# Kernel optimization log

Measured on AMD Instinct MI355X. Metric: run time of the kernel, lower is better.

The kernel has to match this reference:

```python
import jax, jax.numpy as jnp
import numpy as np
from jax import lax

B, T, I = 64, 128, 128   # batch, encoder time, signal features
H = 512                  # lstm hidden size
V = 32                   # vocab = len(output_dict); SOS=0, EOS=1
L = 64                   # decode steps = target_onehot.shape[1]


def lstm_cell(x, h, c, Wih, Whh, bih, bhh):
    # PyTorch gate order: i, f, g, o. x:[B,in], h/c:[B,H]
    g = x @ Wih.T + h @ Whh.T + (bih + bhh)
    i, f, gg, o = jnp.split(g, 4, axis=-1)
    c_new = jax.nn.sigmoid(f) * c + jax.nn.sigmoid(i) * jnp.tanh(gg)
    h_new = jax.nn.sigmoid(o) * jnp.tanh(c_new)
    return h_new, c_new


def setup_inputs() -> dict:
    key = jax.random.key(0)
    ks = jax.random.split(key, 16)
    s = 1.0 / np.sqrt(H)
    u = lambda k, shape: jax.random.uniform(k, shape, jnp.float32, -s, s)
    inp = {}
    inp["signal"] = jax.random.normal(ks[0], (B, T, I), jnp.float32)
    tgt_ids = jax.random.randint(ks[1], (B, L), 0, V)
    inp["target_onehot"] = jax.nn.one_hot(tgt_ids, V, dtype=jnp.float32)
    # encoder bi-LSTM params, stacked [2(dir), ...]
    inp["enc_Wih"] = u(ks[2], (2, 4 * H, I))
    inp["enc_Whh"] = u(ks[3], (2, 4 * H, H))
    inp["enc_bih"] = u(ks[4], (2, 4 * H))
    inp["enc_bhh"] = u(ks[5], (2, 4 * H))
    # decoder bi-LSTM params
    inp["dec_Wih"] = u(ks[6], (2, 4 * H, V))
    inp["dec_Whh"] = u(ks[7], (2, 4 * H, H))
    inp["dec_bih"] = u(ks[8], (2, 4 * H))
    inp["dec_bhh"] = u(ks[9], (2, 4 * H))
    # output projection Linear(2H -> V)
    so = 1.0 / np.sqrt(2 * H)
    inp["W_out"] = jax.random.uniform(ks[10], (V, 2 * H), jnp.float32, -so, so)
    inp["b_out"] = jax.random.uniform(ks[11], (V,), jnp.float32, -so, so)
    return inp


def _forward(signal, target_onehot, enc_Wih, enc_Whh, enc_bih, enc_bhh,
             dec_Wih, dec_Whh, dec_bih, dec_bhh, W_out, b_out):
    Bv = signal.shape[0]
    zeros = jnp.zeros((Bv, H), signal.dtype)
    xs = jnp.swapaxes(signal, 0, 1)  # [T,B,I]

    def enc_step(d):
        def f(carry, x):
            h, c = carry
            h, c = lstm_cell(x, h, c, enc_Wih[d], enc_Whh[d], enc_bih[d], enc_bhh[d])
            return (h, c), None
        return f

    # forward direction final state; backward direction runs on reversed seq
    (hf, cf), _ = lax.scan(enc_step(0), (zeros, zeros), xs)
    (hb, cb), _ = lax.scan(enc_step(1), (zeros, zeros), xs[::-1])

    def dec_step(carry, _):
        inp, hf, cf, hb, cb = carry
        x = jax.nn.relu(inp)  # relu of one-hot (identity, kept for fidelity)
        hf, cf = lstm_cell(x, hf, cf, dec_Wih[0], dec_Whh[0], dec_bih[0], dec_bhh[0])
        hb, cb = lstm_cell(x, hb, cb, dec_Wih[1], dec_Whh[1], dec_bih[1], dec_bhh[1])
        logits = jnp.concatenate([hf, hb], axis=-1) @ W_out.T + b_out  # [B,V]
        # teacher forcing prob is 0 in the source -> always greedy one-hot feedback
        nxt = jax.nn.one_hot(jnp.argmax(logits, axis=-1), V, dtype=logits.dtype)
        return (nxt, hf, cf, hb, cb), logits

    init = (target_onehot[:, 0], hf, cf, hb, cb)
    _, logits = lax.scan(dec_step, init, None, length=target_onehot.shape[1])
    logits = jnp.swapaxes(logits, 0, 1)  # [B,L,V]
    return jax.nn.log_softmax(logits, axis=-1)


def reference(signal, target_onehot, enc_Wih, enc_Whh, enc_bih, enc_bhh,
              dec_Wih, dec_Whh, dec_bih, dec_bhh, W_out, b_out):
    return _forward(signal, target_onehot, enc_Wih, enc_Whh, enc_bih, enc_bhh,
                    dec_Wih, dec_Whh, dec_bih, dec_bhh, W_out, b_out)
```

## Files before the change

### kernel.cpp

```cpp
#include <hip/hip_runtime.h>
#include <math.h>

#define DEV __device__ __forceinline__
typedef __attribute__((ext_vector_type(4))) float f32x4;

constexpr int BATCH = 64;
constexpr int TSTEP = 128;
constexpr int IDIM  = 128;
constexpr int HDIM  = 512;
constexpr int VDIM  = 32;
constexpr int LDEC  = 64;
constexpr int NBLK  = 256;
constexpr int BDIM  = 256;
constexpr unsigned MAGIC = 0x1357BD1u;
constexpr unsigned SPIN_LIMIT = 1u << 22;

constexpr size_t OFF_BAR  = 0;
constexpr size_t OFF_SIGT = 4096;
constexpr size_t OFF_HT   = OFF_SIGT + (size_t)TSTEP*IDIM*BATCH*4;
constexpr size_t OFF_XD   = OFF_HT   + (size_t)2*2*HDIM*BATCH*4;
constexpr size_t WS_NEED  = OFF_XD   + (size_t)VDIM*BATCH*4;


DEV unsigned ldu(const unsigned* p){ return __hip_atomic_load(p, __ATOMIC_RELAXED, __HIP_MEMORY_SCOPE_AGENT); }
DEV void     stu(unsigned* p, unsigned v){ __hip_atomic_store(p, v, __ATOMIC_RELAXED, __HIP_MEMORY_SCOPE_AGENT); }
DEV unsigned fau(unsigned* p, unsigned v){ return __hip_atomic_fetch_add(p, v, __ATOMIC_RELAXED, __HIP_MEMORY_SCOPE_AGENT); }
DEV void     ast(float* p, float v){ __hip_atomic_store(p, v, __ATOMIC_RELAXED, __HIP_MEMORY_SCOPE_AGENT); }
DEV void wait_vm0(){ asm volatile("s_waitcnt vmcnt(0)" ::: "memory"); }
DEV f32x4 gl4_sc1(const float* p){ f32x4 r; asm volatile("global_load_dwordx4 %0, %1, off sc1" : "=v"(r) : "v"(p)); return r; }
DEV f32x4 gl4_pln(const float* p){ f32x4 r; asm volatile("global_load_dwordx4 %0, %1, off"     : "=v"(r) : "v"(p)); return r; }
DEV float gl1_sc1(const float* p){ float r; asm volatile("global_load_dword %0, %1, off sc1"   : "=v"(r) : "v"(p)); return r; }

DEV void spin_ge(const unsigned* p, unsigned tgt, unsigned* dead) {
  unsigned spins = 0;
  while (ldu(p) < tgt) {
    __builtin_amdgcn_s_sleep(1);
    if ((++spins & 255u) == 0u) {
      if (ldu(dead)) break;
      if (spins > SPIN_LIMIT) { stu(dead, 1u); break; }
    }
  }
}

DEV void hbar(unsigned* bar, int gline, int grp, int ngrp, unsigned grpsz, int genline, unsigned* dead) {
  wait_vm0();
  __syncthreads();
  if (threadIdx.x == 0) {
    unsigned* gen = bar + genline*32;
    unsigned g = ldu(gen);
    unsigned* gc = bar + (gline + grp)*32;
    unsigned a = fau(gc, 1u);
    bool rel = false;
    if (a == grpsz - 1u) {
      stu(gc, 0u);
      unsigned* rt = bar + (gline + ngrp)*32;
      unsigned ra = fau(rt, 1u);
      if (ra == (unsigned)ngrp - 1u) { stu(rt, 0u); fau(gen, 1u); rel = true; }
    }
    if (!rel) spin_ge(gen, g + 1u, dead);
  }
  __syncthreads();
}

DEV void gbar_full(unsigned* cnt, unsigned* gen, unsigned nb, unsigned* dead) {
  __syncthreads();
  if (threadIdx.x == 0) {
    unsigned g = ldu(gen);
    unsigned a = __hip_atomic_fetch_add(cnt, 1u, __ATOMIC_ACQ_REL, __HIP_MEMORY_SCOPE_AGENT);
    if (a >= nb - 1u) {
      stu(cnt, 0u);
      __hip_atomic_fetch_add(gen, 1u, __ATOMIC_RELEASE, __HIP_MEMORY_SCOPE_AGENT);
    } else {
      spin_ge(gen, g + 1u, dead);
      (void)__hip_atomic_load(gen, __ATOMIC_ACQUIRE, __HIP_MEMORY_SCOPE_AGENT);
    }
  }
  __syncthreads();
}

template<int KX, bool XSC1>
DEV void cell_step(float acc[4], const float* __restrict__ xsrc,
                   const float* __restrict__ hcur,
                   const float* const* wx, const float* const* wh,
                   int b, int tid, float* __restrict__ buf)
{
  constexpr int  NXC = KX / 64;
  constexpr bool XR  = (KX % 64) != 0;
  constexpr int  NC  = NXC + (XR ? 1 : 0) + HDIM / 64;
  f32x4 r[4];

  auto issue = [&](int c) {
    if (c < NXC) {
      const float* s = xsrc + (size_t)c*4096 + tid*4;
      #pragma unroll
      for (int q = 0; q < 4; ++q) r[q] = XSC1 ? gl4_sc1(s + q*1024) : gl4_pln(s + q*1024);
    } else if (XR && c == NXC) {
      const float* s = xsrc + tid*4;
      #pragma unroll
      for (int q = 0; q < 2; ++q) r[q] = XSC1 ? gl4_sc1(s + q*1024) : gl4_pln(s + q*1024);
    } else {
      const int ch = c - NXC - (XR ? 1 : 0);
      const float* s = hcur + (size_t)ch*4096 + tid*4;
      #pragma unroll
      for (int q = 0; q < 4; ++q) r[q] = gl4_sc1(s + q*1024);
    }
  };

  issue(0);
  for (int c = 0; c < NC; ++c) {
    wait_vm0();
    float* dst = buf + (c & 1)*4096;
    const bool small = (XR && c == NXC);
    *(f32x4*)(dst + tid*4)        = r[0];
    *(f32x4*)(dst + tid*4 + 1024) = r[1];
    if (!small) {
      *(f32x4*)(dst + tid*4 + 2048) = r[2];
      *(f32x4*)(dst + tid*4 + 3072) = r[3];
    }
    __syncthreads();
    if (c + 1 < NC) issue(c + 1);
    const float *g0, *g1, *g2, *g3;
    if (c < NXC)            { g0=wx[0]+c*64; g1=wx[1]+c*64; g2=wx[2]+c*64; g3=wx[3]+c*64; }
    else if (XR && c==NXC)  { g0=wx[0];      g1=wx[1];      g2=wx[2];      g3=wx[3]; }
    else { const int ch=c-NXC-(XR?1:0); g0=wh[0]+ch*64; g1=wh[1]+ch*64; g2=wh[2]+ch*64; g3=wh[3]+ch*64; }
    const float* bs = dst + b;
    if (!small) {
      #pragma unroll
      for (int kk = 0; kk < 64; ++kk) {
        float xv = bs[kk*64];
        acc[0] += g0[kk]*xv; acc[1] += g1[kk]*xv; acc[2] += g2[kk]*xv; acc[3] += g3[kk]*xv;
      }
    } else {
      #pragma unroll
      for (int kk = 0; kk < 32; ++kk) {
        float xv = bs[kk*64];
        acc[0] += g0[kk]*xv; acc[1] += g1[kk]*xv; acc[2] += g2[kk]*xv; acc[3] += g3[kk]*xv;
      }
    }
  }
}

__global__ void __launch_bounds__(BDIM)
encdec(const float* __restrict__ signal, const float* __restrict__ tgt,
       const float* __restrict__ eWih, const float* __restrict__ eWhh,
       const float* __restrict__ eBih, const float* __restrict__ eBhh,
       const float* __restrict__ dWih, const float* __restrict__ dWhh,
       const float* __restrict__ dBih, const float* __restrict__ dBhh,
       const float* __restrict__ Wout, const float* __restrict__ bOut,
       float* __restrict__ out,
       unsigned* __restrict__ bar, float* __restrict__ sigT,
       float* __restrict__ hT, float* __restrict__ xdT)
{
  __shared__ __align__(16) float buf[2*4096];
  __shared__ float red[BDIM];
  const int blk = blockIdx.x, tid = threadIdx.x;
  const int d  = blk >> 7;
  const int js = blk & 127;
  const int b  = tid & 63;
  const int jj = tid >> 6;
  const int j  = js * 4 + jj;

  unsigned* dead = bar + 11*32;
  if (blk == 0 && tid == 0) {
    for (int q = 1; q <= 30; ++q) stu(bar + q*32, 0u);
    __hip_atomic_store(bar, MAGIC, __ATOMIC_RELEASE, __HIP_MEMORY_SCOPE_AGENT);
  }
  if (tid == 0) {
    unsigned spins = 0;
    while (__hip_atomic_load(bar, __ATOMIC_RELAXED, __HIP_MEMORY_SCOPE_AGENT) != MAGIC) {
      __builtin_amdgcn_s_sleep(1);
      if (++spins > SPIN_LIMIT) break;
    }
    (void)__hip_atomic_load(bar, __ATOMIC_ACQUIRE, __HIP_MEMORY_SCOPE_AGENT);
  }
  __syncthreads();

  {
    const int t = blk & 127, ih = blk >> 7;
    float* tile = buf;
    for (int idx = tid; idx < 64*64; idx += BDIM) {
      int il = idx & 63, bb = idx >> 6;
      tile[il*65 + bb] = signal[((size_t)bb*TSTEP + t)*IDIM + ih*64 + il];
    }
    __syncthreads();
    for (int idx = tid; idx < 64*64; idx += BDIM) {
      int bb = idx & 63, il = idx >> 6;
      sigT[((size_t)t*IDIM + ih*64 + il)*64 + bb] = tile[il*65 + bb];
    }
  }
  ast(&hT[((size_t)(0*2 + d)*HDIM + j)*64 + b], 0.f);
  ast(&hT[((size_t)(1*2 + d)*HDIM + j)*64 + b], 0.f);
  if (blk < BATCH && tid < VDIM) {
    float tv = tgt[((size_t)blk*LDEC)*VDIM + tid];
    ast(&xdT[tid*64 + blk], tv > 0.f ? tv : 0.f);
  }
  gbar_full(bar + 29*32, bar + 30*32, NBLK, dead);

  const float* wx[4]; const float* wh[4]; float bsum[4];
  #pragma unroll
  for (int g = 0; g < 4; ++g) {
    int r = __builtin_amdgcn_readfirstlane(g*HDIM + j);
    wx[g] = eWih + ((size_t)d*4*HDIM + r)*IDIM;
    wh[g] = eWhh + ((size_t)d*4*HDIM + r)*HDIM;
    bsum[g] = eBih[d*4*HDIM + r] + eBhh[d*4*HDIM + r];
  }
  float c = 0.f;
  for (int t = 0; t < TSTEP; ++t) {
    const int cur = t & 1, nxt = cur ^ 1;
    const int td = d ? (TSTEP - 1 - t) : t;
    float acc[4] = {0.f, 0.f, 0.f, 0.f};
    cell_step<IDIM, false>(acc, sigT + (size_t)td*IDIM*64,
                           hT + ((size_t)(cur*2 + d)*HDIM)*64, wx, wh, b, tid, buf);
    float gi = acc[0]+bsum[0], gf = acc[1]+bsum[1], gg = acc[2]+bsum[2], go = acc[3]+bsum[3];
    float si = 1.f/(1.f+expf(-gi)), sf = 1.f/(1.f+expf(-gf)), so = 1.f/(1.f+expf(-go));
    c = sf*c + si*tanhf(gg);
    ast(&hT[((size_t)(nxt*2 + d)*HDIM + j)*64 + b], so*tanhf(c));
    hbar(bar, d ? 18 : 12, (blk >> 5) & 3, 4, 32u, d ? 23 : 17, dead);
  }
  hbar(bar, 1, blk & 7, 8, 32u, 10, dead);

  #pragma unroll
  for (int g = 0; g < 4; ++g) {
    int r = __builtin_amdgcn_readfirstlane(g*HDIM + j);
    wx[g] = dWih + ((size_t)d*4*HDIM + r)*VDIM;
    wh[g] = dWhh + ((size_t)d*4*HDIM + r)*HDIM;
    bsum[g] = dBih[d*4*HDIM + r] + dBhh[d*4*HDIM + r];
  }
  for (int s = 0; s < LDEC; ++s) {
    const int cur = s & 1, nxt = cur ^ 1;
    float acc[4] = {0.f, 0.f, 0.f, 0.f};
    cell_step<VDIM, true>(acc, xdT, hT + ((size_t)(cur*2 + d)*HDIM)*64, wx, wh, b, tid, buf);
    float gi = acc[0]+bsum[0], gf = acc[1]+bsum[1], gg = acc[2]+bsum[2], go = acc[3]+bsum[3];
    float si = 1.f/(1.f+expf(-gi)), sf = 1.f/(1.f+expf(-gf)), so = 1.f/(1.f+expf(-go));
    c = sf*c + si*tanhf(gg);
    ast(&hT[((size_t)(nxt*2 + d)*HDIM + j)*64 + b], so*tanhf(c));
    hbar(bar, 1, blk & 7, 8, 32u, 10, dead);

    if (blk < BATCH) {
      const int bb = blk, v = tid & 31, kc = tid >> 5;
      const float* hx = hT + (size_t)nxt*2*HDIM*64 + bb;
      float part = 0.f;
      float rr[32];
      for (int w = 0; w < 4; ++w) {
        #pragma unroll
        for (int i = 0; i < 32; ++i)
          rr[i] = gl1_sc1(hx + (size_t)(kc*128 + w*32 + i)*64);
        wait_vm0();
        #pragma unroll
        for (int i = 0; i < 32; ++i)
          part += Wout[(size_t)v*(2*HDIM) + kc*128 + w*32 + i] * rr[i];
      }
      red[tid] = part;
      __syncthreads();
      if (tid < VDIM) {
        float lg = red[tid];
        #pragma unroll
        for (int q = 1; q < 8; ++q) lg += red[tid + q*32];
        lg += bOut[tid];
        float m = lg; int mi = tid;
        #pragma unroll
        for (int off = 16; off >= 1; off >>= 1) {
          float om = __shfl_xor(m, off, 64);
          int omi  = __shfl_xor(mi, off, 64);
          if (om > m || (om == m && omi < mi)) { m = om; mi = omi; }
        }
        float ex = expf(lg - m), ssum = ex;
        #pragma unroll
        for (int off = 16; off >= 1; off >>= 1) ssum += __shfl_xor(ssum, off, 64);
        out[((size_t)bb*LDEC + s)*VDIM + tid] = lg - m - logf(ssum);
        ast(&xdT[tid*64 + bb], (tid == mi) ? 1.f : 0.f);
      }
    }
    hbar(bar, 1, blk & 7, 8, 32u, 10, dead);
  }
}

extern "C" void kernel_launch(void* const* d_in, const int* in_sizes, int n_in,
                              void* d_out, int out_size, void* d_ws, size_t ws_size,
                              hipStream_t stream) {
  if (ws_size < WS_NEED) return;
  char* base = (char*)d_ws;
  hipLaunchKernelGGL(encdec, dim3(NBLK), dim3(BDIM), 0, stream,
    (const float*)d_in[0],  (const float*)d_in[1],
    (const float*)d_in[2],  (const float*)d_in[3],
    (const float*)d_in[4],  (const float*)d_in[5],
    (const float*)d_in[6],  (const float*)d_in[7],
    (const float*)d_in[8],  (const float*)d_in[9],
    (const float*)d_in[10], (const float*)d_in[11],
    (float*)d_out,
    (unsigned*)(base + OFF_BAR), (float*)(base + OFF_SIGT),
    (float*)(base + OFF_HT),     (float*)(base + OFF_XD));
}
```

Before: 4.670 ms.

## Stage per-block LSTM weight slices in LDS and shrink staging chunks

Each block now copies its 16 gate rows of the input and recurrent weights (encoder, then decoder) into shared memory once, with a padded stride. The inner loop then reads weights as vectorized LDS loads instead of per-step global loads through wave-uniform pointers. The input/hidden staging chunk is cut from 64 to 32 k-values, which halves the double buffer and doubles the number of chunk iterations and __syncthreads per step. Shared memory use grows to about 57 KB, which costs one-time copy work and may limit residency.

Result: faster. 4.157 ms (-11.0%).

```diff
diff --git a/kernel.cpp b/kernel.cpp
--- a/kernel.cpp
+++ b/kernel.cpp
@@ -14,6 +14,10 @@
 constexpr int BDIM  = 256;
 constexpr unsigned MAGIC = 0x1357BD1u;
 constexpr unsigned SPIN_LIMIT = 1u << 22;
+
+constexpr int WS_E = 644;
+constexpr int WS_D = 548;
+constexpr int SM_BUF = 0, SM_W = 4096, SM_RED = 4096 + 10304, SM_TOT = 14656;
 
 constexpr size_t OFF_BAR  = 0;
 constexpr size_t OFF_SIGT = 4096;
@@ -78,64 +82,42 @@
   __syncthreads();
 }
 
-template<int KX, bool XSC1>
+template<int KX, int WS, bool XSC1>
 DEV void cell_step(float acc[4], const float* __restrict__ xsrc,
-                   const float* __restrict__ hcur,
-                   const float* const* wx, const float* const* wh,
-                   int b, int tid, float* __restrict__ buf)
+                   const float* __restrict__ hcur, const float* __restrict__ Wl,
+                   int b, int jj, int tid, float* __restrict__ buf)
 {
-  constexpr int  NXC = KX / 64;
-  constexpr bool XR  = (KX % 64) != 0;
-  constexpr int  NC  = NXC + (XR ? 1 : 0) + HDIM / 64;
-  f32x4 r[4];
-
+  constexpr int NXC = KX / 32;
+  constexpr int NC  = NXC + HDIM / 32;
+  f32x4 r0, r1;
   auto issue = [&](int c) {
-    if (c < NXC) {
-      const float* s = xsrc + (size_t)c*4096 + tid*4;
-      #pragma unroll
-      for (int q = 0; q < 4; ++q) r[q] = XSC1 ? gl4_sc1(s + q*1024) : gl4_pln(s + q*1024);
-    } else if (XR && c == NXC) {
-      const float* s = xsrc + tid*4;
-      #pragma unroll
-      for (int q = 0; q < 2; ++q) r[q] = XSC1 ? gl4_sc1(s + q*1024) : gl4_pln(s + q*1024);
-    } else {
-      const int ch = c - NXC - (XR ? 1 : 0);
-      const float* s = hcur + (size_t)ch*4096 + tid*4;
-      #pragma unroll
-      for (int q = 0; q < 4; ++q) r[q] = gl4_sc1(s + q*1024);
-    }
+    const float* s = (c < NXC) ? xsrc + (size_t)c*2048 + tid*8
+                               : hcur + (size_t)(c - NXC)*2048 + tid*8;
+    if (c < NXC && !XSC1) { r0 = gl4_pln(s); r1 = gl4_pln(s + 4); }
+    else                  { r0 = gl4_sc1(s); r1 = gl4_sc1(s + 4); }
   };
-
   issue(0);
   for (int c = 0; c < NC; ++c) {
     wait_vm0();
-    float* dst = buf + (c & 1)*4096;
-    const bool small = (XR && c == NXC);
-    *(f32x4*)(dst + tid*4)        = r[0];
-    *(f32x4*)(dst + tid*4 + 1024) = r[1];
-    if (!small) {
-      *(f32x4*)(dst + tid*4 + 2048) = r[2];
-      *(f32x4*)(dst + tid*4 + 3072) = r[3];
-    }
+    float* dst = buf + (c & 1)*2048;
+    *(f32x4*)(dst + tid*8)     = r0;
+    *(f32x4*)(dst + tid*8 + 4) = r1;
     __syncthreads();
     if (c + 1 < NC) issue(c + 1);
-    const float *g0, *g1, *g2, *g3;
-    if (c < NXC)            { g0=wx[0]+c*64; g1=wx[1]+c*64; g2=wx[2]+c*64; g3=wx[3]+c*64; }
-    else if (XR && c==NXC)  { g0=wx[0];      g1=wx[1];      g2=wx[2];      g3=wx[3]; }
-    else { const int ch=c-NXC-(XR?1:0); g0=wh[0]+ch*64; g1=wh[1]+ch*64; g2=wh[2]+ch*64; g3=wh[3]+ch*64; }
+    const float* wr = Wl + (size_t)(jj*4)*WS + c*32;
     const float* bs = dst + b;
-    if (!small) {
-      #pragma unroll
-      for (int kk = 0; kk < 64; ++kk) {
-        float xv = bs[kk*64];
-        acc[0] += g0[kk]*xv; acc[1] += g1[kk]*xv; acc[2] += g2[kk]*xv; acc[3] += g3[kk]*xv;
-      }
-    } else {
-      #pragma unroll
-      for (int kk = 0; kk < 32; ++kk) {
-        float xv = bs[kk*64];
-        acc[0] += g0[kk]*xv; acc[1] += g1[kk]*xv; acc[2] += g2[kk]*xv; acc[3] += g3[kk]*xv;
-      }
+    #pragma unroll
+    for (int kq = 0; kq < 8; ++kq) {
+      f32x4 w0 = *(const f32x4*)(wr + 0*WS + kq*4);
+      f32x4 w1 = *(const f32x4*)(wr + 1*WS + kq*4);
+      f32x4 w2 = *(const f32x4*)(wr + 2*WS + kq*4);
+      f32x4 w3 = *(const f32x4*)(wr + 3*WS + kq*4);
+      float x0 = bs[(kq*4+0)*64], x1 = bs[(kq*4+1)*64];
+      float x2 = bs[(kq*4+2)*64], x3 = bs[(kq*4+3)*64];
+      acc[0] += w0[0]*x0 + w0[1]*x1 + w0[2]*x2 + w0[3]*x3;
+      acc[1] += w1[0]*x0 + w1[1]*x1 + w1[2]*x2 + w1[3]*x3;
+      acc[2] += w2[0]*x0 + w2[1]*x1 + w2[2]*x2 + w2[3]*x3;
+      acc[3] += w3[0]*x0 + w3[1]*x1 + w3[2]*x2 + w3[3]*x3;
     }
   }
 }
@@ -151,8 +133,10 @@
        unsigned* __restrict__ bar, float* __restrict__ sigT,
        float* __restrict__ hT, float* __restrict__ xdT)
 {
-  __shared__ __align__(16) float buf[2*4096];
-  __shared__ float red[BDIM];
+  __shared__ __align__(16) float smem[SM_TOT];
+  float* buf = smem + SM_BUF;
+  float* Wl  = smem + SM_W;
+  float* red = smem + SM_RED;
   const int blk = blockIdx.x, tid = threadIdx.x;
   const int d  = blk >> 7;
   const int js = blk & 127;
@@ -177,7 +161,7 @@
 
   {
     const int t = blk & 127, ih = blk >> 7;
-    float* tile = buf;
+    float* tile = smem;
     for (int idx = tid; idx < 64*64; idx += BDIM) {
       int il = idx & 63, bb = idx >> 6;
       tile[il*65 + bb] = signal[((size_t)bb*TSTEP + t)*IDIM + ih*64 + il];
@@ -187,6 +171,14 @@
       int bb = idx & 63, il = idx >> 6;
       sigT[((size_t)t*IDIM + ih*64 + il)*64 + bb] = tile[il*65 + bb];
     }
+    __syncthreads();
+  }
+  for (int idx = tid; idx < 16*640; idx += BDIM) {
+    int row = idx / 640, k = idx - row*640;
+    int g = row & 3, ju = row >> 2;
+    int r = d*4*HDIM + g*HDIM + (js*4 + ju);
+    Wl[(size_t)row*WS_E + k] = (k < IDIM) ? eWih[(size_t)r*IDIM + k]
+                                          : eWhh[(size_t)r*HDIM + (k - IDIM)];
   }
   ast(&hT[((size_t)(0*2 + d)*HDIM + j)*64 + b], 0.f);
   ast(&hT[((size_t)(1*2 + d)*HDIM + j)*64 + b], 0.f);
@@ -196,21 +188,19 @@
   }
   gbar_full(bar + 29*32, bar + 30*32, NBLK, dead);
 
-  const float* wx[4]; const float* wh[4]; float bsum[4];
+  float bsum[4];
   #pragma unroll
   for (int g = 0; g < 4; ++g) {
-    int r = __builtin_amdgcn_readfirstlane(g*HDIM + j);
-    wx[g] = eWih + ((size_t)d*4*HDIM + r)*IDIM;
-    wh[g] = eWhh + ((size_t)d*4*HDIM + r)*HDIM;
-    bsum[g] = eBih[d*4*HDIM + r] + eBhh[d*4*HDIM + r];
+    int r = __builtin_amdgcn_readfirstlane(d*4*HDIM + g*HDIM + j);
+    bsum[g] = eBih[r] + eBhh[r];
   }
   float c = 0.f;
   for (int t = 0; t < TSTEP; ++t) {
     const int cur = t & 1, nxt = cur ^ 1;
     const int td = d ? (TSTEP - 1 - t) : t;
     float acc[4] = {0.f, 0.f, 0.f, 0.f};
-    cell_step<IDIM, false>(acc, sigT + (size_t)td*IDIM*64,
-                           hT + ((size_t)(cur*2 + d)*HDIM)*64, wx, wh, b, tid, buf);
+    cell_step<IDIM, WS_E, false>(acc, sigT + (size_t)td*IDIM*64,
+                                 hT + ((size_t)(cur*2 + d)*HDIM)*64, Wl, b, jj, tid, buf);
     float gi = acc[0]+bsum[0], gf = acc[1]+bsum[1], gg = acc[2]+bsum[2], go = acc[3]+bsum[3];
     float si = 1.f/(1.f+expf(-gi)), sf = 1.f/(1.f+expf(-gf)), so = 1.f/(1.f+expf(-go));
     c = sf*c + si*tanhf(gg);
@@ -219,17 +209,25 @@
   }
   hbar(bar, 1, blk & 7, 8, 32u, 10, dead);
 
+  for (int idx = tid; idx < 16*544; idx += BDIM) {
+    int row = idx / 544, k = idx - row*544;
+    int g = row & 3, ju = row >> 2;
+    int r = d*4*HDIM + g*HDIM + (js*4 + ju);
+    Wl[(size_t)row*WS_D + k] = (k < VDIM) ? dWih[(size_t)r*VDIM + k]
+                                          : dWhh[(size_t)r*HDIM + (k - VDIM)];
+  }
   #pragma unroll
   for (int g = 0; g < 4; ++g) {
-    int r = __builtin_amdgcn_readfirstlane(g*HDIM + j);
-    wx[g] = dWih + ((size_t)d*4*HDIM + r)*VDIM;
-    wh[g] = dWhh + ((size_t)d*4*HDIM + r)*HDIM;
-    bsum[g] = dBih[d*4*HDIM + r] + dBhh[d*4*HDIM + r];
-  }
+    int r = __builtin_amdgcn_readfirstlane(d*4*HDIM + g*HDIM + j);
+    bsum[g] = dBih[r] + dBhh[r];
+  }
+  __syncthreads();
+
   for (int s = 0; s < LDEC; ++s) {
     const int cur = s & 1, nxt = cur ^ 1;
     float acc[4] = {0.f, 0.f, 0.f, 0.f};
-    cell_step<VDIM, true>(acc, xdT, hT + ((size_t)(cur*2 + d)*HDIM)*64, wx, wh, b, tid, buf);
+    cell_step<VDIM, WS_D, true>(acc, xdT, hT + ((size_t)(cur*2 + d)*HDIM)*64,
+                                Wl, b, jj, tid, buf);
     float gi = acc[0]+bsum[0], gf = acc[1]+bsum[1], gg = acc[2]+bsum[2], go = acc[3]+bsum[3];
     float si = 1.f/(1.f+expf(-gi)), sf = 1.f/(1.f+expf(-gf)), so = 1.f/(1.f+expf(-go));
     c = sf*c + si*tanhf(gg);
```
